# Performance work log

Hardware: AMD Instinct MI355X
Metric: run time of the kernel (lower is better)

The kernel has to match this reference:

```python
import jax, jax.numpy as jnp
import numpy as np

D_MODEL = 256
NHEAD = 8
DK = D_MODEL // NHEAD
EDGE_FEAT_DIM = 7
N_NODES = 2048
N_EDGES = 65536
LN_EPS = 1e-5


def _ln(x, g, b):
    mu = jnp.mean(x, axis=-1, keepdims=True)
    var = jnp.mean(jnp.square(x - mu), axis=-1, keepdims=True)
    return (x - mu) * jax.lax.rsqrt(var + LN_EPS) * g + b


def setup_inputs() -> dict:
    key = jax.random.key(0)
    ks = jax.random.split(key, 16)
    d, h2 = D_MODEL, 2 * D_MODEL
    s = 0.02
    inp = {
        "h": jax.random.normal(ks[0], (N_NODES, d), jnp.float32),
        "edge_attr": jax.random.normal(ks[1], (N_EDGES, EDGE_FEAT_DIM), jnp.float32),
        # weights stored as (in, out): y = x @ W + b (matches torch Linear math)
        "Wq": s * jax.random.normal(ks[2], (d, d), jnp.float32),
        "bq": jnp.zeros((d,), jnp.float32),
        "Wk": s * jax.random.normal(ks[3], (d, d), jnp.float32),
        "bk": jnp.zeros((d,), jnp.float32),
        "Wv": s * jax.random.normal(ks[4], (d, d), jnp.float32),
        "bv": jnp.zeros((d,), jnp.float32),
        "Wo": s * jax.random.normal(ks[5], (d, d), jnp.float32),
        "bo": jnp.zeros((d,), jnp.float32),
        "We": s * jax.random.normal(ks[6], (EDGE_FEAT_DIM, NHEAD), jnp.float32),
        "be": jnp.zeros((NHEAD,), jnp.float32),
        "ln1_g": jnp.ones((d,), jnp.float32),
        "ln1_b": jnp.zeros((d,), jnp.float32),
        "fln_g": jnp.ones((d,), jnp.float32),
        "fln_b": jnp.zeros((d,), jnp.float32),
        "W1": s * jax.random.normal(ks[7], (d, h2), jnp.float32),
        "b1": jnp.zeros((h2,), jnp.float32),
        "W2": s * jax.random.normal(ks[8], (h2, d), jnp.float32),
        "b2": jnp.zeros((d,), jnp.float32),
        "edge_index": jax.random.randint(ks[9], (2, N_EDGES), 0, N_NODES, jnp.int64 if jax.config.jax_enable_x64 else jnp.int32),
    }
    return inp


def reference(h, edge_attr, Wq, bq, Wk, bk, Wv, bv, Wo, bo, We, be,
              ln1_g, ln1_b, fln_g, fln_b, W1, b1, W2, b2, edge_index):
    N = h.shape[0]
    res = h
    # edge bias scattered into dense (N, N, H) tensor
    eb = edge_attr @ We + be                                  # (E, H)
    attn_bias = jnp.zeros((N, N, NHEAD), h.dtype).at[edge_index[0], edge_index[1]].set(eb)
    Q = (h @ Wq + bq).reshape(N, NHEAD, DK)
    K = (h @ Wk + bk).reshape(N, NHEAD, DK)
    V = (h @ Wv + bv).reshape(N, NHEAD, DK)
    scores = jnp.einsum('nhd,mhd->nmh', Q, K) / jnp.sqrt(jnp.float32(DK)) + attn_bias
    attn = jax.nn.softmax(scores, axis=1)                     # softmax over keys m
    out = jnp.einsum('nmh,mhd->nhd', attn, V).reshape(N, D_MODEL)
    out = out @ Wo + bo
    h1 = _ln(res + out, ln1_g, ln1_b)
    ffn = jax.nn.gelu(_ln(h1, fln_g, fln_b) @ W1 + b1, approximate=False) @ W2 + b2
    return h1 + ffn
```

## Files before the change

### kernel.cpp

```cpp
#include <hip/hip_runtime.h>
#include <math.h>

#define NN 2048
#define NE 65536
#define DM 256
#define NH 8
#define DKH 32
#define CAP 128
#define TM2 128
#define SPLIT 4

typedef __attribute__((ext_vector_type(8))) short bf16x8;
typedef __attribute__((ext_vector_type(4))) float f32x4;

__device__ __forceinline__ unsigned short f2b(float f) {
    unsigned u = __float_as_uint(f);
    unsigned r = (u + 0x7FFFu + ((u >> 16) & 1u)) >> 16;
    return (unsigned short)r;
}
__device__ __forceinline__ float b2f(unsigned short s) {
    return __uint_as_float(((unsigned)s) << 16);
}

__global__ __launch_bounds__(256) void edge_prep_kernel(
    const float* __restrict__ ea, const float* __restrict__ We,
    const float* __restrict__ be, const int* __restrict__ ei,
    float* __restrict__ eb, int* __restrict__ cnt, int* __restrict__ lst)
{
    int e = blockIdx.x * 256 + threadIdx.x;
    float acc[NH];
#pragma unroll
    for (int h = 0; h < NH; ++h) acc[h] = be[h];
#pragma unroll
    for (int f = 0; f < 7; ++f) {
        float x = ea[e * 7 + f];
#pragma unroll
        for (int h = 0; h < NH; ++h) acc[h] = fmaf(x, We[f * NH + h], acc[h]);
    }
#pragma unroll
    for (int h = 0; h < NH; ++h) eb[e * NH + h] = acc[h];
    int s = ei[e];
    int p = atomicAdd(&cnt[s], 1);
    if (p < CAP) lst[s * CAP + p] = e;
}

__global__ __launch_bounds__(128) void rowprep_kernel(
    const int* __restrict__ ei, const int* __restrict__ cnt,
    const int* __restrict__ lst, int* __restrict__ sortedDest,
    int* __restrict__ sortedE, int* __restrict__ rowOff)
{
    __shared__ int ds[CAP], es[CAP];
    __shared__ int bc[16], off[17];
    int n = blockIdx.x, t = threadIdx.x;
    int c = cnt[n]; if (c > CAP) c = CAP;
    if (t < 16) bc[t] = 0;
    int e = -1, d = -1;
    if (t < c) { e = lst[n * CAP + t]; d = ei[NE + e]; }
    ds[t] = d; es[t] = e;
    __syncthreads();
    bool win = (t < c);
    if (win) {
        for (int j = 0; j < c; ++j)
            if (ds[j] == d && es[j] > e) { win = false; break; }
    }
    int bkt = (d >= 0) ? (d >> 7) : 0;
    int pos = -1;
    if (win) pos = atomicAdd(&bc[bkt], 1);
    __syncthreads();
    if (t == 0) {
        int s = 0;
        for (int i = 0; i < 16; ++i) { off[i] = s; s += bc[i]; }
        off[16] = s;
    }
    __syncthreads();
    if (win) {
        int p = off[bkt] + pos;
        sortedDest[n * CAP + p] = d;
        sortedE[n * CAP + p] = e;
    }
    if (t < 17) rowOff[n * 17 + t] = off[t];
}

__global__ __launch_bounds__(256) void prep_kernel(
    const float* __restrict__ h, const float* __restrict__ Wq,
    const float* __restrict__ Wk, const float* __restrict__ Wv,
    const float* __restrict__ Wo, const float* __restrict__ W1,
    const float* __restrict__ W2,
    unsigned short* __restrict__ hb, unsigned short* __restrict__ Wqkvt,
    unsigned short* __restrict__ Wot, unsigned short* __restrict__ W1t,
    unsigned short* __restrict__ W2t)
{
    int i = blockIdx.x * 256 + threadIdx.x;
    if (i < 524288) {
        hb[i] = f2b(h[i]);
    } else if (i < 720896) {
        int j = i - 524288;
        int n = j >> 8, k = j & 255;
        const float* W = (n < 256) ? Wq : (n < 512) ? Wk : Wv;
        Wqkvt[j] = f2b(W[k * 256 + (n & 255)]);
    } else if (i < 786432) {
        int j = i - 720896;
        int n = j >> 8, k = j & 255;
        Wot[j] = f2b(Wo[k * 256 + n]);
    } else if (i < 917504) {
        int j = i - 786432;
        int n = j >> 8, k = j & 255;
        W1t[j] = f2b(W1[(size_t)k * 512 + n]);
    } else {
        int j = i - 917504;
        int n = j >> 9, k = j & 511;
        W2t[j] = f2b(W2[(size_t)k * 256 + n]);
    }
}

template <int EPI, int MT>
__global__ __launch_bounds__(MT * 4) void gemm_bf16(
    const unsigned short* __restrict__ A, const unsigned short* __restrict__ Bt,
    const float* __restrict__ bias0, const float* __restrict__ bias1,
    const float* __restrict__ bias2, const float* __restrict__ resid,
    void* __restrict__ out0, void* __restrict__ out1, void* __restrict__ out2,
    int M, int N, int K)
{
    __shared__ unsigned short As[MT][40];
    __shared__ unsigned short Bs[64][40];
    int tid = threadIdx.x;
    int wv = tid >> 6, l = tid & 63, l15 = l & 15, quad = l >> 4;
    int m0 = blockIdx.y * MT, n0 = blockIdx.x * 64;

    f32x4 acc[4];
#pragma unroll
    for (int i = 0; i < 4; ++i) acc[i] = (f32x4){0.f, 0.f, 0.f, 0.f};

    int ra = tid >> 2, ka = (tid & 3) * 8;

    for (int k0 = 0; k0 < K; k0 += 32) {
        *(uint4*)&As[ra][ka] = *(const uint4*)(A + (size_t)(m0 + ra) * K + k0 + ka);
        if (MT == 64) {
            *(uint4*)&Bs[ra][ka] = *(const uint4*)(Bt + (size_t)(n0 + ra) * K + k0 + ka);
        } else {
            int rb = tid >> 1, kb = (tid & 1) * 16;
            *(uint4*)&Bs[rb][kb]     = *(const uint4*)(Bt + (size_t)(n0 + rb) * K + k0 + kb);
            *(uint4*)&Bs[rb][kb + 8] = *(const uint4*)(Bt + (size_t)(n0 + rb) * K + k0 + kb + 8);
        }
        __syncthreads();
        bf16x8 a = *(const bf16x8*)&As[wv * 16 + l15][quad * 8];
#pragma unroll
        for (int nt = 0; nt < 4; ++nt) {
            bf16x8 b = *(const bf16x8*)&Bs[nt * 16 + l15][quad * 8];
            acc[nt] = __builtin_amdgcn_mfma_f32_16x16x32_bf16(a, b, acc[nt], 0, 0, 0);
        }
        __syncthreads();
    }

#pragma unroll
    for (int nt = 0; nt < 4; ++nt) {
#pragma unroll
        for (int r = 0; r < 4; ++r) {
            int row = m0 + wv * 16 + quad * 4 + r;
            int col = n0 + nt * 16 + l15;
            float v = acc[nt][r];
            if (EPI == 0) {
                v += bias0[col];
                if (resid) v += resid[(size_t)row * N + col];
                ((float*)out0)[(size_t)row * N + col] = v;
            } else if (EPI == 1) {
                v += bias0[col];
                v = 0.5f * v * (1.0f + erff(v * 0.70710678118654752f));
                ((unsigned short*)out0)[(size_t)row * N + col] = f2b(v);
            } else {
                if (col < 256) {
                    v = (v + bias0[col]) * 0.17677669529663689f;
                    ((unsigned short*)out0)[(size_t)row * 256 + col] = f2b(v);
                } else if (col < 512) {
                    v += bias1[col - 256];
                    ((unsigned short*)out1)[(size_t)row * 256 + col - 256] = f2b(v);
                } else {
                    v += bias2[col - 512];
                    ((unsigned short*)out2)[(size_t)row * 256 + col - 512] = f2b(v);
                }
            }
        }
    }
}

__global__ __launch_bounds__(256) void vtrans_kernel(
    const unsigned short* __restrict__ Vb, unsigned short* __restrict__ Vt)
{
    __shared__ unsigned short tile[64][40];
    int h = blockIdx.y, n0 = blockIdx.x * 64, t = threadIdx.x;
    int r = t >> 2, c8 = (t & 3) * 8;
    *(uint4*)&tile[r][c8] = *(const uint4*)(Vb + (size_t)(n0 + r) * DM + h * 32 + c8);
    __syncthreads();
    int d = t >> 3, nc = (t & 7) * 8;
    unsigned short o[8];
#pragma unroll
    for (int j = 0; j < 8; ++j) o[j] = tile[nc + j][d];
    *(uint4*)(Vt + ((size_t)h * 32 + d) * NN + n0 + nc) = *(uint4*)o;
}

__global__ __launch_bounds__(256) void attn_mfma(
    const unsigned short* __restrict__ Qb, const unsigned short* __restrict__ Kb,
    const unsigned short* __restrict__ Vt, const float* __restrict__ eb,
    const int* __restrict__ sortedDest, const int* __restrict__ sortedE,
    const int* __restrict__ rowOff,
    float* __restrict__ accD, float* __restrict__ lD)
{
    __shared__ unsigned short Ks[TM2][40];
    __shared__ unsigned short Vs[32][TM2 + 8];
    __shared__ unsigned short Ps[4][16][TM2 + 16];
    __shared__ float ldelta[4][16];
    int h = blockIdx.y, tid = threadIdx.x;
    int wv = tid >> 6, l = tid & 63, l15 = l & 15, quad = l >> 4;
    int n0 = blockIdx.x * 64 + wv * 16;
    int mz = blockIdx.z;

    if (l < 16) ldelta[wv][l] = 0.f;

    bf16x8 aq = *(const bf16x8*)(Qb + (size_t)(n0 + l15) * DM + h * 32 + quad * 8);

    f32x4 oacc[2];
    oacc[0] = (f32x4){0.f, 0.f, 0.f, 0.f};
    oacc[1] = (f32x4){0.f, 0.f, 0.f, 0.f};
    float lacc[4] = {0.f, 0.f, 0.f, 0.f};
    const unsigned short* Vth = Vt + (size_t)h * 32 * NN;

    int r16 = l >> 2, sub = l & 3;
    int frow = n0 + r16;

    for (int t = 0; t < NN / (TM2 * SPLIT); ++t) {
        int m0 = (mz * (NN / SPLIT)) + t * TM2;
        int ti = m0 >> 7;
        {
            int r = tid >> 1, kc = (tid & 1) * 16;
            const unsigned short* ks = Kb + (size_t)(m0 + r) * DM + h * 32 + kc;
            *(uint4*)&Ks[r][kc]     = *(const uint4*)(ks);
            *(uint4*)&Ks[r][kc + 8] = *(const uint4*)(ks + 8);
            int d = tid >> 3, mc = (tid & 7) * 16;
            const unsigned short* vs = Vth + (size_t)d * NN + m0 + mc;
            *(uint4*)&Vs[d][mc]     = *(const uint4*)(vs);
            *(uint4*)&Vs[d][mc + 8] = *(const uint4*)(vs + 8);
        }
        __syncthreads();
#pragma unroll
        for (int mt = 0; mt < TM2 / 16; ++mt) {
            bf16x8 bk = *(const bf16x8*)&Ks[mt * 16 + l15][quad * 8];
            f32x4 s = __builtin_amdgcn_mfma_f32_16x16x32_bf16(
                aq, bk, (f32x4){0.f, 0.f, 0.f, 0.f}, 0, 0, 0);
#pragma unroll
            for (int r = 0; r < 4; ++r) {
                float p = __expf(s[r]);
                lacc[r] += p;
                Ps[wv][quad * 4 + r][mt * 16 + l15] = f2b(p);
            }
        }
        __syncthreads();
        {
            int o0 = rowOff[frow * 17 + ti];
            int o1 = rowOff[frow * 17 + ti + 1];
            for (int idx = o0 + sub; idx < o1; idx += 4) {
                int d = sortedDest[frow * CAP + idx] - m0;
                int e = sortedE[frow * CAP + idx];
                float expb = __expf(eb[e * NH + h]);
                float pold = b2f(Ps[wv][r16][d]);
                Ps[wv][r16][d] = f2b(pold * expb);
                atomicAdd(&ldelta[wv][r16], pold * (expb - 1.0f));
            }
        }
        __syncthreads();
#pragma unroll
        for (int kc = 0; kc < TM2 / 32; ++kc) {
            bf16x8 ap = *(const bf16x8*)&Ps[wv][l15][kc * 32 + quad * 8];
#pragma unroll
            for (int nt = 0; nt < 2; ++nt) {
                bf16x8 bv = *(const bf16x8*)&Vs[nt * 16 + l15][kc * 32 + quad * 8];
                oacc[nt] = __builtin_amdgcn_mfma_f32_16x16x32_bf16(ap, bv, oacc[nt], 0, 0, 0);
            }
        }
        __syncthreads();
    }

#pragma unroll
    for (int off = 1; off < 16; off <<= 1) {
#pragma unroll
        for (int r = 0; r < 4; ++r) lacc[r] += __shfl_xor(lacc[r], off);
    }
    float* lDp = lD + (size_t)mz * NN * NH;
    if (l15 == 0) {
#pragma unroll
        for (int r = 0; r < 4; ++r)
            lDp[(size_t)(n0 + quad * 4 + r) * NH + h] = lacc[r] + ldelta[wv][quad * 4 + r];
    }
    float* aDp = accD + (size_t)mz * NN * DM;
#pragma unroll
    for (int nt = 0; nt < 2; ++nt)
#pragma unroll
        for (int r = 0; r < 4; ++r)
            aDp[(size_t)(n0 + quad * 4 + r) * DM + h * 32 + nt * 16 + l15] = oacc[nt][r];
}

__global__ __launch_bounds__(256) void norm_kernel(
    const float* __restrict__ accD, const float* __restrict__ lD,
    unsigned short* __restrict__ AOb)
{
    int i = blockIdx.x * 256 + threadIdx.x;
    int n = i >> 8, cdim = i & 255, h = cdim >> 5;
    float o = 0.f, lsum = 0.f;
#pragma unroll
    for (int s = 0; s < SPLIT; ++s) {
        o += accD[(size_t)s * NN * DM + i];
        lsum += lD[(size_t)s * NN * NH + (size_t)n * NH + h];
    }
    AOb[i] = f2b(o / lsum);
}

__global__ __launch_bounds__(256) void ln2_kernel(
    const float* __restrict__ T, const float* __restrict__ g1, const float* __restrict__ b1,
    const float* __restrict__ g2, const float* __restrict__ b2,
    float* __restrict__ H1, unsigned short* __restrict__ X2b)
{
    __shared__ float red[4];
    int n = blockIdx.x, t = threadIdx.x;
    float x = T[(size_t)n * DM + t];

    float s = x;
#pragma unroll
    for (int off = 32; off; off >>= 1) s += __shfl_xor(s, off);
    if ((t & 63) == 0) red[t >> 6] = s;
    __syncthreads();
    float mu = (red[0] + red[1] + red[2] + red[3]) * (1.0f / 256.0f);
    __syncthreads();

    float d = x - mu;
    float v = d * d;
#pragma unroll
    for (int off = 32; off; off >>= 1) v += __shfl_xor(v, off);
    if ((t & 63) == 0) red[t >> 6] = v;
    __syncthreads();
    float var = (red[0] + red[1] + red[2] + red[3]) * (1.0f / 256.0f);
    float y = d * rsqrtf(var + 1e-5f) * g1[t] + b1[t];
    H1[(size_t)n * DM + t] = y;
    __syncthreads();

    float s2 = y;
#pragma unroll
    for (int off = 32; off; off >>= 1) s2 += __shfl_xor(s2, off);
    if ((t & 63) == 0) red[t >> 6] = s2;
    __syncthreads();
    float mu2 = (red[0] + red[1] + red[2] + red[3]) * (1.0f / 256.0f);
    __syncthreads();

    float d2 = y - mu2;
    float v2 = d2 * d2;
#pragma unroll
    for (int off = 32; off; off >>= 1) v2 += __shfl_xor(v2, off);
    if ((t & 63) == 0) red[t >> 6] = v2;
    __syncthreads();
    float var2 = (red[0] + red[1] + red[2] + red[3]) * (1.0f / 256.0f);
    X2b[(size_t)n * DM + t] = f2b(d2 * rsqrtf(var2 + 1e-5f) * g2[t] + b2[t]);
}

extern "C" void kernel_launch(void* const* d_in, const int* in_sizes, int n_in,
                              void* d_out, int out_size, void* d_ws, size_t ws_size,
                              hipStream_t stream)
{
    const float* h    = (const float*)d_in[0];
    const float* ea   = (const float*)d_in[1];
    const float* Wq   = (const float*)d_in[2];
    const float* bq   = (const float*)d_in[3];
    const float* Wk   = (const float*)d_in[4];
    const float* bk   = (const float*)d_in[5];
    const float* Wv   = (const float*)d_in[6];
    const float* bv   = (const float*)d_in[7];
    const float* Wo   = (const float*)d_in[8];
    const float* bo   = (const float*)d_in[9];
    const float* We   = (const float*)d_in[10];
    const float* be   = (const float*)d_in[11];
    const float* ln1g = (const float*)d_in[12];
    const float* ln1b = (const float*)d_in[13];
    const float* flng = (const float*)d_in[14];
    const float* flnb = (const float*)d_in[15];
    const float* W1   = (const float*)d_in[16];
    const float* b1   = (const float*)d_in[17];
    const float* W2   = (const float*)d_in[18];
    const float* b2   = (const float*)d_in[19];
    const int*   ei   = (const int*)d_in[20];
    float* out = (float*)d_out;

    char* p = (char*)d_ws;
    float* eb   = (float*)p;           p += (size_t)NE * NH * 4;
    int*   cnt  = (int*)p;             p += (size_t)NN * 4;
    int*   lst  = (int*)p;             p += (size_t)NN * CAP * 4;
    int*   sD   = (int*)p;             p += (size_t)NN * CAP * 4;
    int*   sE   = (int*)p;             p += (size_t)NN * CAP * 4;
    int*   rOff = (int*)p;             p += (size_t)NN * 17 * 4;
    unsigned short* hb    = (unsigned short*)p; p += (size_t)NN * DM * 2;
    unsigned short* Wqkvt = (unsigned short*)p; p += (size_t)768 * 256 * 2;
    unsigned short* Wot   = (unsigned short*)p; p += (size_t)256 * 256 * 2;
    unsigned short* W1t   = (unsigned short*)p; p += (size_t)512 * 256 * 2;
    unsigned short* W2t   = (unsigned short*)p; p += (size_t)256 * 512 * 2;
    unsigned short* Qb    = (unsigned short*)p; p += (size_t)NN * DM * 2;
    unsigned short* Kb    = (unsigned short*)p; p += (size_t)NN * DM * 2;
    unsigned short* Vb    = (unsigned short*)p; p += (size_t)NN * DM * 2;
    unsigned short* Vt    = (unsigned short*)p; p += (size_t)NN * DM * 2;
    float* accD = (float*)p;           p += (size_t)SPLIT * NN * DM * 4;
    float* lD   = (float*)p;           p += (size_t)SPLIT * NN * NH * 4;
    unsigned short* AOb   = (unsigned short*)p; p += (size_t)NN * DM * 2;
    float* T    = (float*)p;           p += (size_t)NN * DM * 4;
    float* H1   = (float*)p;           p += (size_t)NN * DM * 4;
    unsigned short* X2b   = (unsigned short*)p; p += (size_t)NN * DM * 2;
    unsigned short* F1b   = (unsigned short*)p; p += (size_t)NN * 512 * 2;

    hipMemsetAsync(cnt, 0, (size_t)NN * 4, stream);
    edge_prep_kernel<<<NE / 256, 256, 0, stream>>>(ea, We, be, ei, eb, cnt, lst);
    rowprep_kernel<<<NN, 128, 0, stream>>>(ei, cnt, lst, sD, sE, rOff);

    prep_kernel<<<1048576 / 256, 256, 0, stream>>>(
        h, Wq, Wk, Wv, Wo, W1, W2, hb, Wqkvt, Wot, W1t, W2t);

    gemm_bf16<2, 64><<<dim3(768 / 64, NN / 64), 256, 0, stream>>>(
        hb, Wqkvt, bq, bk, bv, nullptr, Qb, Kb, Vb, NN, 768, 256);
    vtrans_kernel<<<dim3(NN / 64, NH), 256, 0, stream>>>(Vb, Vt);

    attn_mfma<<<dim3(NN / 64, NH, SPLIT), 256, 0, stream>>>(
        Qb, Kb, Vt, eb, sD, sE, rOff, accD, lD);
    norm_kernel<<<NN * DM / 256, 256, 0, stream>>>(accD, lD, AOb);

    gemm_bf16<0, 32><<<dim3(256 / 64, NN / 32), 128, 0, stream>>>(
        AOb, Wot, bo, nullptr, nullptr, h, T, nullptr, nullptr, NN, 256, 256);
    ln2_kernel<<<NN, 256, 0, stream>>>(T, ln1g, ln1b, flng, flnb, H1, X2b);

    gemm_bf16<1, 64><<<dim3(512 / 64, NN / 64), 256, 0, stream>>>(
        X2b, W1t, b1, nullptr, nullptr, nullptr, F1b, nullptr, nullptr, NN, 512, 256);
    gemm_bf16<0, 32><<<dim3(256 / 64, NN / 32), 128, 0, stream>>>(
        F1b, W2t, b2, nullptr, nullptr, H1, out, nullptr, nullptr, NN, 256, 512);
}
```

Measured before the change: 189.0 us.

## Fuse prep kernels, use exp2 softmax, wave-local P sync, fuse Wo+LN

Result: faster. 179.0 us (-5.3%).

```diff
diff --git a/kernel.cpp b/kernel.cpp
--- a/kernel.cpp
+++ b/kernel.cpp
@@ -13,6 +13,8 @@
 typedef __attribute__((ext_vector_type(8))) short bf16x8;
 typedef __attribute__((ext_vector_type(4))) float f32x4;
 
+#define WAVE_LDS_SYNC() __asm__ volatile("s_waitcnt lgkmcnt(0)" ::: "memory")
+
 __device__ __forceinline__ unsigned short f2b(float f) {
     unsigned u = __float_as_uint(f);
     unsigned r = (u + 0x7FFFu + ((u >> 16) & 1u)) >> 16;
@@ -22,26 +24,59 @@
     return __uint_as_float(((unsigned)s) << 16);
 }
 
-__global__ __launch_bounds__(256) void edge_prep_kernel(
-    const float* __restrict__ ea, const float* __restrict__ We,
-    const float* __restrict__ be, const int* __restrict__ ei,
-    float* __restrict__ eb, int* __restrict__ cnt, int* __restrict__ lst)
-{
-    int e = blockIdx.x * 256 + threadIdx.x;
-    float acc[NH];
-#pragma unroll
-    for (int h = 0; h < NH; ++h) acc[h] = be[h];
-#pragma unroll
-    for (int f = 0; f < 7; ++f) {
-        float x = ea[e * 7 + f];
-#pragma unroll
-        for (int h = 0; h < NH; ++h) acc[h] = fmaf(x, We[f * NH + h], acc[h]);
-    }
-#pragma unroll
-    for (int h = 0; h < NH; ++h) eb[e * NH + h] = acc[h];
-    int s = ei[e];
-    int p = atomicAdd(&cnt[s], 1);
-    if (p < CAP) lst[s * CAP + p] = e;
+__global__ __launch_bounds__(256) void prep_all_kernel(
+    const float* __restrict__ h, const float* __restrict__ Wq,
+    const float* __restrict__ Wk, const float* __restrict__ Wv,
+    const float* __restrict__ Wo, const float* __restrict__ W1,
+    const float* __restrict__ W2, const float* __restrict__ ea,
+    const float* __restrict__ We, const float* __restrict__ be,
+    const int* __restrict__ ei,
+    unsigned short* __restrict__ hb, unsigned short* __restrict__ Wqkvt,
+    unsigned short* __restrict__ Wot, unsigned short* __restrict__ W1t,
+    unsigned short* __restrict__ W2t, float* __restrict__ eb,
+    int* __restrict__ cnt, int* __restrict__ lst)
+{
+    int b = blockIdx.x;
+    if (b < 4096) {
+        int i = b * 256 + threadIdx.x;
+        if (i < 524288) {
+            hb[i] = f2b(h[i]);
+        } else if (i < 720896) {
+            int j = i - 524288;
+            int n = j >> 8, k = j & 255;
+            const float* W = (n < 256) ? Wq : (n < 512) ? Wk : Wv;
+            Wqkvt[j] = f2b(W[k * 256 + (n & 255)]);
+        } else if (i < 786432) {
+            int j = i - 720896;
+            int n = j >> 8, k = j & 255;
+            Wot[j] = f2b(Wo[k * 256 + n]);
+        } else if (i < 917504) {
+            int j = i - 786432;
+            int n = j >> 8, k = j & 255;
+            W1t[j] = f2b(W1[(size_t)k * 512 + n]);
+        } else {
+            int j = i - 917504;
+            int n = j >> 9, k = j & 511;
+            W2t[j] = f2b(W2[(size_t)k * 256 + n]);
+        }
+    } else {
+        int e = (b - 4096) * 256 + threadIdx.x;
+        float acc[NH];
+#pragma unroll
+        for (int hh = 0; hh < NH; ++hh) acc[hh] = be[hh];
+#pragma unroll
+        for (int f = 0; f < 7; ++f) {
+            float x = ea[e * 7 + f];
+#pragma unroll
+            for (int hh = 0; hh < NH; ++hh) acc[hh] = fmaf(x, We[f * NH + hh], acc[hh]);
+        }
+#pragma unroll
+        for (int hh = 0; hh < NH; ++hh)
+            eb[e * NH + hh] = acc[hh] * 1.44269504088896f;
+        int s = ei[e];
+        int p = atomicAdd(&cnt[s], 1);
+        if (p < CAP) lst[s * CAP + p] = e;
+    }
 }
 
 __global__ __launch_bounds__(128) void rowprep_kernel(
@@ -79,38 +114,6 @@
         sortedE[n * CAP + p] = e;
     }
     if (t < 17) rowOff[n * 17 + t] = off[t];
-}
-
-__global__ __launch_bounds__(256) void prep_kernel(
-    const float* __restrict__ h, const float* __restrict__ Wq,
-    const float* __restrict__ Wk, const float* __restrict__ Wv,
-    const float* __restrict__ Wo, const float* __restrict__ W1,
-    const float* __restrict__ W2,
-    unsigned short* __restrict__ hb, unsigned short* __restrict__ Wqkvt,
-    unsigned short* __restrict__ Wot, unsigned short* __restrict__ W1t,
-    unsigned short* __restrict__ W2t)
-{
-    int i = blockIdx.x * 256 + threadIdx.x;
-    if (i < 524288) {
-        hb[i] = f2b(h[i]);
-    } else if (i < 720896) {
-        int j = i - 524288;
-        int n = j >> 8, k = j & 255;
-        const float* W = (n < 256) ? Wq : (n < 512) ? Wk : Wv;
-        Wqkvt[j] = f2b(W[k * 256 + (n & 255)]);
-    } else if (i < 786432) {
-        int j = i - 720896;
-        int n = j >> 8, k = j & 255;
-        Wot[j] = f2b(Wo[k * 256 + n]);
-    } else if (i < 917504) {
-        int j = i - 786432;
-        int n = j >> 8, k = j & 255;
-        W1t[j] = f2b(W1[(size_t)k * 512 + n]);
-    } else {
-        int j = i - 917504;
-        int n = j >> 9, k = j & 511;
-        W2t[j] = f2b(W2[(size_t)k * 256 + n]);
-    }
 }
 
 template <int EPI, int MT>
@@ -169,7 +172,7 @@
                 ((unsigned short*)out0)[(size_t)row * N + col] = f2b(v);
             } else {
                 if (col < 256) {
-                    v = (v + bias0[col]) * 0.17677669529663689f;
+                    v = (v + bias0[col]) * 0.2550348592f;
                     ((unsigned short*)out0)[(size_t)row * 256 + col] = f2b(v);
                 } else if (col < 512) {
                     v += bias1[col - 256];
@@ -205,9 +208,9 @@
     const int* __restrict__ rowOff,
     float* __restrict__ accD, float* __restrict__ lD)
 {
-    __shared__ unsigned short Ks[TM2][40];
-    __shared__ unsigned short Vs[32][TM2 + 8];
-    __shared__ unsigned short Ps[4][16][TM2 + 16];
+    __shared__ __align__(16) unsigned short Ks[TM2][40];
+    __shared__ __align__(16) unsigned short Vs[32][TM2 + 8];
+    __shared__ __align__(16) unsigned short Pn[4][16][TM2 + 16];
     __shared__ float ldelta[4][16];
     int h = blockIdx.y, tid = threadIdx.x;
     int wv = tid >> 6, l = tid & 63, l15 = l & 15, quad = l >> 4;
@@ -221,7 +224,7 @@
     f32x4 oacc[2];
     oacc[0] = (f32x4){0.f, 0.f, 0.f, 0.f};
     oacc[1] = (f32x4){0.f, 0.f, 0.f, 0.f};
-    float lacc[4] = {0.f, 0.f, 0.f, 0.f};
+    float lacc = 0.f;
     const unsigned short* Vth = Vt + (size_t)h * 32 * NN;
 
     int r16 = l >> 2, sub = l & 3;
@@ -243,33 +246,35 @@
         __syncthreads();
 #pragma unroll
         for (int mt = 0; mt < TM2 / 16; ++mt) {
-            bf16x8 bk = *(const bf16x8*)&Ks[mt * 16 + l15][quad * 8];
+            bf16x8 ak = *(const bf16x8*)&Ks[mt * 16 + l15][quad * 8];
             f32x4 s = __builtin_amdgcn_mfma_f32_16x16x32_bf16(
-                aq, bk, (f32x4){0.f, 0.f, 0.f, 0.f}, 0, 0, 0);
-#pragma unroll
-            for (int r = 0; r < 4; ++r) {
-                float p = __expf(s[r]);
-                lacc[r] += p;
-                Ps[wv][quad * 4 + r][mt * 16 + l15] = f2b(p);
-            }
-        }
-        __syncthreads();
+                ak, aq, (f32x4){0.f, 0.f, 0.f, 0.f}, 0, 0, 0);
+            float p0 = __builtin_amdgcn_exp2f(s[0]);
+            float p1 = __builtin_amdgcn_exp2f(s[1]);
+            float p2 = __builtin_amdgcn_exp2f(s[2]);
+            float p3 = __builtin_amdgcn_exp2f(s[3]);
+            lacc += (p0 + p1) + (p2 + p3);
+            unsigned u0 = (unsigned)f2b(p0) | ((unsigned)f2b(p1) << 16);
+            unsigned u1 = (unsigned)f2b(p2) | ((unsigned)f2b(p3) << 16);
+            *(uint2*)&Pn[wv][l15][mt * 16 + quad * 4] = (uint2){u0, u1};
+        }
+        WAVE_LDS_SYNC();
         {
             int o0 = rowOff[frow * 17 + ti];
             int o1 = rowOff[frow * 17 + ti + 1];
             for (int idx = o0 + sub; idx < o1; idx += 4) {
                 int d = sortedDest[frow * CAP + idx] - m0;
                 int e = sortedE[frow * CAP + idx];
-                float expb = __expf(eb[e * NH + h]);
-                float pold = b2f(Ps[wv][r16][d]);
-                Ps[wv][r16][d] = f2b(pold * expb);
+                float expb = __builtin_amdgcn_exp2f(eb[e * NH + h]);
+                float pold = b2f(Pn[wv][r16][d]);
+                Pn[wv][r16][d] = f2b(pold * expb);
                 atomicAdd(&ldelta[wv][r16], pold * (expb - 1.0f));
             }
         }
-        __syncthreads();
+        WAVE_LDS_SYNC();
 #pragma unroll
         for (int kc = 0; kc < TM2 / 32; ++kc) {
-            bf16x8 ap = *(const bf16x8*)&Ps[wv][l15][kc * 32 + quad * 8];
+            bf16x8 ap = *(const bf16x8*)&Pn[wv][l15][kc * 32 + quad * 8];
 #pragma unroll
             for (int nt = 0; nt < 2; ++nt) {
                 bf16x8 bv = *(const bf16x8*)&Vs[nt * 16 + l15][kc * 32 + quad * 8];
@@ -279,17 +284,11 @@
         __syncthreads();
     }
 
-#pragma unroll
-    for (int off = 1; off < 16; off <<= 1) {
-#pragma unroll
-        for (int r = 0; r < 4; ++r) lacc[r] += __shfl_xor(lacc[r], off);
-    }
+    lacc += __shfl_xor(lacc, 16);
+    lacc += __shfl_xor(lacc, 32);
     float* lDp = lD + (size_t)mz * NN * NH;
-    if (l15 == 0) {
-#pragma unroll
-        for (int r = 0; r < 4; ++r)
-            lDp[(size_t)(n0 + quad * 4 + r) * NH + h] = lacc[r] + ldelta[wv][quad * 4 + r];
-    }
+    if (l < 16)
+        lDp[(size_t)(n0 + l) * NH + h] = lacc + ldelta[wv][l];
     float* aDp = accD + (size_t)mz * NN * DM;
 #pragma unroll
     for (int nt = 0; nt < 2; ++nt)
@@ -298,65 +297,114 @@
             aDp[(size_t)(n0 + quad * 4 + r) * DM + h * 32 + nt * 16 + l15] = oacc[nt][r];
 }
 
-__global__ __launch_bounds__(256) void norm_kernel(
+__global__ __launch_bounds__(256) void wo_ln_kernel(
     const float* __restrict__ accD, const float* __restrict__ lD,
-    unsigned short* __restrict__ AOb)
-{
-    int i = blockIdx.x * 256 + threadIdx.x;
-    int n = i >> 8, cdim = i & 255, h = cdim >> 5;
-    float o = 0.f, lsum = 0.f;
-#pragma unroll
-    for (int s = 0; s < SPLIT; ++s) {
-        o += accD[(size_t)s * NN * DM + i];
-        lsum += lD[(size_t)s * NN * NH + (size_t)n * NH + h];
-    }
-    AOb[i] = f2b(o / lsum);
-}
-
-__global__ __launch_bounds__(256) void ln2_kernel(
-    const float* __restrict__ T, const float* __restrict__ g1, const float* __restrict__ b1,
-    const float* __restrict__ g2, const float* __restrict__ b2,
-    float* __restrict__ H1, unsigned short* __restrict__ X2b)
-{
-    __shared__ float red[4];
-    int n = blockIdx.x, t = threadIdx.x;
-    float x = T[(size_t)n * DM + t];
-
-    float s = x;
-#pragma unroll
-    for (int off = 32; off; off >>= 1) s += __shfl_xor(s, off);
-    if ((t & 63) == 0) red[t >> 6] = s;
-    __syncthreads();
-    float mu = (red[0] + red[1] + red[2] + red[3]) * (1.0f / 256.0f);
-    __syncthreads();
-
-    float d = x - mu;
-    float v = d * d;
-#pragma unroll
-    for (int off = 32; off; off >>= 1) v += __shfl_xor(v, off);
-    if ((t & 63) == 0) red[t >> 6] = v;
-    __syncthreads();
-    float var = (red[0] + red[1] + red[2] + red[3]) * (1.0f / 256.0f);
-    float y = d * rsqrtf(var + 1e-5f) * g1[t] + b1[t];
-    H1[(size_t)n * DM + t] = y;
-    __syncthreads();
-
-    float s2 = y;
-#pragma unroll
-    for (int off = 32; off; off >>= 1) s2 += __shfl_xor(s2, off);
-    if ((t & 63) == 0) red[t >> 6] = s2;
-    __syncthreads();
-    float mu2 = (red[0] + red[1] + red[2] + red[3]) * (1.0f / 256.0f);
-    __syncthreads();
-
-    float d2 = y - mu2;
-    float v2 = d2 * d2;
-#pragma unroll
-    for (int off = 32; off; off >>= 1) v2 += __shfl_xor(v2, off);
-    if ((t & 63) == 0) red[t >> 6] = v2;
-    __syncthreads();
-    float var2 = (red[0] + red[1] + red[2] + red[3]) * (1.0f / 256.0f);
-    X2b[(size_t)n * DM + t] = f2b(d2 * rsqrtf(var2 + 1e-5f) * g2[t] + b2[t]);
+    const unsigned short* __restrict__ Wot, const float* __restrict__ bo,
+    const float* __restrict__ h, const float* __restrict__ g1,
+    const float* __restrict__ b1, const float* __restrict__ g2,
+    const float* __restrict__ b2, float* __restrict__ H1,
+    unsigned short* __restrict__ X2b)
+{
+    __shared__ float linv[16][8];
+    __shared__ __align__(16) unsigned short As[16][264];
+    __shared__ __align__(16) unsigned short Bs[256][40];
+    __shared__ float Tt[16][264];
+    __shared__ unsigned short X2s[16][264];
+    int tid = threadIdx.x, m0 = blockIdx.x * 16;
+    int wv = tid >> 6, l = tid & 63, l15 = l & 15, quad = l >> 4;
+
+    if (tid < 128) {
+        int r = tid >> 3, hh = tid & 7;
+        float ls = 0.f;
+#pragma unroll
+        for (int s = 0; s < SPLIT; ++s)
+            ls += lD[(size_t)s * NN * NH + (size_t)(m0 + r) * NH + hh];
+        linv[r][hh] = 1.0f / ls;
+    }
+    __syncthreads();
+#pragma unroll
+    for (int ch = 0; ch < 16; ++ch) {
+        float o = 0.f;
+#pragma unroll
+        for (int s = 0; s < SPLIT; ++s)
+            o += accD[(size_t)s * NN * DM + (size_t)(m0 + ch) * DM + tid];
+        As[ch][tid] = f2b(o * linv[ch][tid >> 5]);
+    }
+    __syncthreads();
+
+    f32x4 acc[4];
+#pragma unroll
+    for (int i = 0; i < 4; ++i) acc[i] = (f32x4){0.f, 0.f, 0.f, 0.f};
+
+    for (int k0 = 0; k0 < 256; k0 += 32) {
+#pragma unroll
+        for (int ps = 0; ps < 4; ++ps) {
+            int row = ps * 64 + (tid >> 2), kk = (tid & 3) * 8;
+            *(uint4*)&Bs[row][kk] = *(const uint4*)(Wot + (size_t)row * 256 + k0 + kk);
+        }
+        __syncthreads();
+        bf16x8 a = *(const bf16x8*)&As[l15][k0 + quad * 8];
+#pragma unroll
+        for (int nt = 0; nt < 4; ++nt) {
+            bf16x8 b = *(const bf16x8*)&Bs[wv * 64 + nt * 16 + l15][quad * 8];
+            acc[nt] = __builtin_amdgcn_mfma_f32_16x16x32_bf16(a, b, acc[nt], 0, 0, 0);
+        }
+        __syncthreads();
+    }
+
+#pragma unroll
+    for (int nt = 0; nt < 4; ++nt)
+#pragma unroll
+        for (int r = 0; r < 4; ++r) {
+            int row = quad * 4 + r, col = wv * 64 + nt * 16 + l15;
+            Tt[row][col] = acc[nt][r] + bo[col] + h[(size_t)(m0 + row) * DM + col];
+        }
+    __syncthreads();
+
+    int rr = tid >> 4, l16 = tid & 15;
+    float x[16];
+#pragma unroll
+    for (int j = 0; j < 16; ++j) x[j] = Tt[rr][l16 + 16 * j];
+    float mu = 0.f;
+#pragma unroll
+    for (int j = 0; j < 16; ++j) mu += x[j];
+#pragma unroll
+    for (int off = 1; off < 16; off <<= 1) mu += __shfl_xor(mu, off);
+    mu *= (1.0f / 256.0f);
+    float var = 0.f;
+#pragma unroll
+    for (int j = 0; j < 16; ++j) { float d = x[j] - mu; var += d * d; }
+#pragma unroll
+    for (int off = 1; off < 16; off <<= 1) var += __shfl_xor(var, off);
+    float rs = rsqrtf(var * (1.0f / 256.0f) + 1e-5f);
+    float y[16]; float mu2 = 0.f;
+#pragma unroll
+    for (int j = 0; j < 16; ++j) {
+        int c = l16 + 16 * j;
+        y[j] = (x[j] - mu) * rs * g1[c] + b1[c];
+        mu2 += y[j];
+    }
+#pragma unroll
+    for (int off = 1; off < 16; off <<= 1) mu2 += __shfl_xor(mu2, off);
+    mu2 *= (1.0f / 256.0f);
+    float var2 = 0.f;
+#pragma unroll
+    for (int j = 0; j < 16; ++j) { float d = y[j] - mu2; var2 += d * d; }
+#pragma unroll
+    for (int off = 1; off < 16; off <<= 1) var2 += __shfl_xor(var2, off);
+    float rs2 = rsqrtf(var2 * (1.0f / 256.0f) + 1e-5f);
+#pragma unroll
+    for (int j = 0; j < 16; ++j) {
+        int c = l16 + 16 * j;
+        Tt[rr][c] = y[j];
+        X2s[rr][c] = f2b((y[j] - mu2) * rs2 * g2[c] + b2[c]);
+    }
+    __syncthreads();
+#pragma unroll
+    for (int ch = 0; ch < 16; ++ch) {
+        H1[(size_t)(m0 + ch) * DM + tid] = Tt[ch][tid];
+        X2b[(size_t)(m0 + ch) * DM + tid] = X2s[ch][tid];
+    }
 }
 
 extern "C" void kernel_launch(void* const* d_in, const int* in_sizes, int n_in,
@@ -404,18 +452,15 @@
     unsigned short* Vt    = (unsigned short*)p; p += (size_t)NN * DM * 2;
     float* accD = (float*)p;           p += (size_t)SPLIT * NN * DM * 4;
     float* lD   = (float*)p;           p += (size_t)SPLIT * NN * NH * 4;
-    unsigned short* AOb   = (unsigned short*)p; p += (size_t)NN * DM * 2;
-    float* T    = (float*)p;           p += (size_t)NN * DM * 4;
     float* H1   = (float*)p;           p += (size_t)NN * DM * 4;
     unsigned short* X2b   = (unsigned short*)p; p += (size_t)NN * DM * 2;
     unsigned short* F1b   = (unsigned short*)p; p += (size_t)NN * 512 * 2;
 
     hipMemsetAsync(cnt, 0, (size_t)NN * 4, stream);
-    edge_prep_kernel<<<NE / 256, 256, 0, stream>>>(ea, We, be, ei, eb, cnt, lst);
+    prep_all_kernel<<<4096 + NE / 256, 256, 0, stream>>>(
+        h, Wq, Wk, Wv, Wo, W1, W2, ea, We, be, ei,
+        hb, Wqkvt, Wot, W1t, W2t, eb, cnt, lst);
     rowprep_kernel<<<NN, 128, 0, stream>>>(ei, cnt, lst, sD, sE, rOff);
-
-    prep_kernel<<<1048576 / 256, 256, 0, stream>>>(
-        h, Wq, Wk, Wv, Wo, W1, W2, hb, Wqkvt, Wot, W1t, W2t);
 
     gemm_bf16<2, 64><<<dim3(768 / 64, NN / 64), 256, 0, stream>>>(
         hb, Wqkvt, bq, bk, bv, nullptr, Qb, Kb, Vb, NN, 768, 256);
@@ -423,11 +468,9 @@
 
     attn_mfma<<<dim3(NN / 64, NH, SPLIT), 256, 0, stream>>>(
         Qb, Kb, Vt, eb, sD, sE, rOff, accD, lD);
-    norm_kernel<<<NN * DM / 256, 256, 0, stream>>>(accD, lD, AOb);
-
-    gemm_bf16<0, 32><<<dim3(256 / 64, NN / 32), 128, 0, stream>>>(
-        AOb, Wot, bo, nullptr, nullptr, h, T, nullptr, nullptr, NN, 256, 256);
-    ln2_kernel<<<NN, 256, 0, stream>>>(T, ln1g, ln1b, flng, flnb, H1, X2b);
+
+    wo_ln_kernel<<<NN / 16, 256, 0, stream>>>(
+        accD, lD, Wot, bo, h, ln1g, ln1b, flng, flnb, H1, X2b);
 
     gemm_bf16<1, 64><<<dim3(512 / 64, NN / 64), 256, 0, stream>>>(
         X2b, W1t, b1, nullptr, nullptr, nullptr, F1b, nullptr, nullptr, NN, 512, 256);
```
